# Kernel tuning notes

Measured on AMD Instinct MI355X. Metric: run time of the kernel, lower is better.

The kernel has to match this reference:

```python
import jax, jax.numpy as jnp
import numpy as np

D_MODEL, N_HEAD, D_FFN = 1024, 16, 4096
MAX_REL = 128
NUM_BUCKETS = 2 * MAX_REL - 1  # 255
B, T = 2, 2048


def algebraic_ln(x, gamma, beta, a, b_raw, eps=1e-5):
    mean = jnp.mean(x, axis=-1, keepdims=True)
    var = jnp.var(x, axis=-1, keepdims=True)  # unbiased=False
    z = var + eps
    b = jax.nn.softplus(10.0 * b_raw) / 10.0  # softplus with beta=10
    p = a[0] + a[1] * z + a[2] * z ** 2
    q = b[0] + b[1] * z + b[2] * z ** 2
    return (x - mean) * (p / q) * gamma + beta


def setup_inputs() -> dict:
    key = jax.random.key(0)
    ks = jax.random.split(key, 16)
    s = (1.0 / np.sqrt(D_MODEL)).astype(np.float32)
    inp = {
        'x': jax.random.normal(ks[0], (B, T, D_MODEL), jnp.float32),
        'casual_mask': jnp.tril(jnp.ones((T, T), dtype=bool)),
        'Wq': jax.random.normal(ks[1], (D_MODEL, D_MODEL), jnp.float32) * s,
        'bq': jnp.zeros((D_MODEL,), jnp.float32),
        'Wk': jax.random.normal(ks[2], (D_MODEL, D_MODEL), jnp.float32) * s,
        'bk': jnp.zeros((D_MODEL,), jnp.float32),
        'Wv': jax.random.normal(ks[3], (D_MODEL, D_MODEL), jnp.float32) * s,
        'bv': jnp.zeros((D_MODEL,), jnp.float32),
        'Wo': jax.random.normal(ks[4], (D_MODEL, D_MODEL), jnp.float32) * s,
        'bo': jnp.zeros((D_MODEL,), jnp.float32),
        'rel_emb': jax.random.normal(ks[5], (NUM_BUCKETS, N_HEAD), jnp.float32) * 0.02,
        'g1': jnp.ones((D_MODEL,), jnp.float32),
        'be1': jnp.zeros((D_MODEL,), jnp.float32),
        'a1': jnp.array([1.0, 0.5, 0.1], jnp.float32),
        'br1': jnp.array([1.0, 0.3, 0.05], jnp.float32),
        'g2': jnp.ones((D_MODEL,), jnp.float32),
        'be2': jnp.zeros((D_MODEL,), jnp.float32),
        'a2': jnp.array([1.0, 0.5, 0.1], jnp.float32),
        'br2': jnp.array([1.0, 0.3, 0.05], jnp.float32),
        'W1': jax.random.normal(ks[6], (D_FFN, D_MODEL), jnp.float32) * s,
        'b1': jnp.zeros((D_FFN,), jnp.float32),
        'W2': jax.random.normal(ks[7], (D_MODEL, D_FFN), jnp.float32) * (1.0 / np.sqrt(D_FFN)),
        'b2': jnp.zeros((D_MODEL,), jnp.float32),
        'res_scale': jnp.array(0.5, jnp.float32),
    }
    return inp


def attention(x, mask, Wq, bq, Wk, bk, Wv, bv, Wo, bo, rel_emb):
    Bx, Tx, C = x.shape
    H, Dh = N_HEAD, C // N_HEAD
    scale = Dh ** -0.5
    Q = (x @ Wq.T + bq).reshape(Bx, Tx, H, Dh)
    K = (x @ Wk.T + bk).reshape(Bx, Tx, H, Dh)
    V = (x @ Wv.T + bv).reshape(Bx, Tx, H, Dh)
    scores = jnp.einsum('bqhd,bkhd->bhqk', Q, K) * scale
    rel = jnp.arange(Tx)[None, :] - jnp.arange(Tx)[:, None]  # k_pos - q_pos
    buckets = jnp.clip(rel, -MAX_REL + 1, MAX_REL - 1) + (MAX_REL - 1)
    bias = rel_emb[buckets]  # [T,T,H]
    scores = scores + jnp.transpose(bias, (2, 0, 1))[None]
    m = mask[None, None]  # [1,1,T,T]
    # torch: masked_fill(-inf) then masked_fill(0) -> masked entries become 0
    scores = jnp.where(m, scores, 0.0)
    w = jax.nn.relu(scores) + 1e-6
    w = jnp.where(m, w, 0.0)
    w = w / (jnp.sum(w, axis=-1, keepdims=True) + 1e-6)
    out = jnp.einsum('bhqk,bkhd->bqhd', w, V).reshape(Bx, Tx, C)
    return out @ Wo.T + bo


def reference(x, casual_mask, Wq, bq, Wk, bk, Wv, bv, Wo, bo, rel_emb,
              g1, be1, a1, br1, g2, be2, a2, br2, W1, b1, W2, b2, res_scale):
    scale = jnp.clip(res_scale, 0.2, 1.0)
    x = x + scale * attention(algebraic_ln(x, g1, be1, a1, br1), casual_mask,
                              Wq, bq, Wk, bk, Wv, bv, Wo, bo, rel_emb)
    h = algebraic_ln(x, g2, be2, a2, br2)
    ffn = jax.nn.relu(h @ W1.T + b1) @ W2.T + b2  # dropout is identity at eval
    return x + scale * ffn
```

## Files before the change

kernel.cpp:

```cpp
#include <hip/hip_runtime.h>
#include <stdint.h>


#define D_MODEL 1024
#define T_SEQ   2048
#define NHEAD   16
#define DH      64
#define DFFN    4096
#define MROWS   4096

using short8  = __attribute__((ext_vector_type(8))) short;
using floatx4 = __attribute__((ext_vector_type(4))) float;

__device__ __forceinline__ float bf2f(ushort u) {
    union { uint32_t i; float f; } x; x.i = ((uint32_t)u) << 16; return x.f;
}
__device__ __forceinline__ ushort f2bf(float f) {
    union { float f; uint32_t i; } x; x.f = f;
    uint32_t i = x.i;
    return (ushort)((i + 0x7fffu + ((i >> 16) & 1u)) >> 16);
}
__device__ __forceinline__ float ldf(const void* p, size_t i, int dt) {
    return dt ? bf2f(((const ushort*)p)[i]) : ((const float*)p)[i];
}
__device__ __forceinline__ int detect_bf16(const void* g1) {
    return *(const uint32_t*)g1 == 0x3F803F80u;
}
__device__ __forceinline__ void gld_lds16(const void* g, void* l) {
    __builtin_amdgcn_global_load_lds(
        (__attribute__((address_space(1))) uint32_t*)(g),
        (__attribute__((address_space(3))) uint32_t*)(l), 16, 0, 0);
}
__device__ __forceinline__ float softplus10(float t) {
    float u = 10.f * t;
    return (u > 20.f ? u : log1pf(expf(u))) * 0.1f;
}

template <int INMODE>
__global__ __launch_bounds__(256)
void ln_kernel(const void* __restrict__ xin,
               const void* __restrict__ gamma, const void* __restrict__ beta,
               const void* __restrict__ a3, const void* __restrict__ br3,
               ushort* __restrict__ out, const void* __restrict__ dtprobe)
{
    const int dt = detect_bf16(dtprobe);
    const int row = blockIdx.x;
    const int tid = threadIdx.x;
    const int col = tid * 4;
    float v[4];
    if (INMODE == 1) {
        const float* x = (const float*)xin + (size_t)row * D_MODEL;
        float4 t = *(const float4*)(x + col);
        v[0] = t.x; v[1] = t.y; v[2] = t.z; v[3] = t.w;
    } else if (dt) {
        const ushort* x = (const ushort*)xin + (size_t)row * D_MODEL;
        ushort4 t = *(const ushort4*)(x + col);
        v[0] = bf2f(t.x); v[1] = bf2f(t.y); v[2] = bf2f(t.z); v[3] = bf2f(t.w);
    } else {
        const float* x = (const float*)xin + (size_t)row * D_MODEL;
        float4 t = *(const float4*)(x + col);
        v[0] = t.x; v[1] = t.y; v[2] = t.z; v[3] = t.w;
    }
    float s  = v[0] + v[1] + v[2] + v[3];
    float s2 = v[0]*v[0] + v[1]*v[1] + v[2]*v[2] + v[3]*v[3];
#pragma unroll
    for (int m = 32; m > 0; m >>= 1) {
        s  += __shfl_down(s,  m, 64);
        s2 += __shfl_down(s2, m, 64);
    }
    __shared__ float wsum[4], wsum2[4];
    const int wave = tid >> 6, lane = tid & 63;
    if (lane == 0) { wsum[wave] = s; wsum2[wave] = s2; }
    __syncthreads();
    s  = wsum[0] + wsum[1] + wsum[2] + wsum[3];
    s2 = wsum2[0] + wsum2[1] + wsum2[2] + wsum2[3];
    const float mean = s * (1.f / D_MODEL);
    const float var  = s2 * (1.f / D_MODEL) - mean * mean;
    const float z = var + 1e-5f;
    const float a0 = ldf(a3, 0, dt), a1 = ldf(a3, 1, dt), a2 = ldf(a3, 2, dt);
    const float b0 = softplus10(ldf(br3, 0, dt));
    const float b1 = softplus10(ldf(br3, 1, dt));
    const float b2 = softplus10(ldf(br3, 2, dt));
    const float p = a0 + a1 * z + a2 * z * z;
    const float q = b0 + b1 * z + b2 * z * z;
    const float f = p / q;
    ushort4 o; ushort* op = (ushort*)&o;
#pragma unroll
    for (int e = 0; e < 4; e++) {
        op[e] = f2bf((v[e] - mean) * f * ldf(gamma, col + e, dt) + ldf(beta, col + e, dt));
    }
    *(ushort4*)(out + (size_t)row * D_MODEL + col) = o;
}

template <int MODE, int BM, int BN>
__global__ __launch_bounds__(256)
void gemm_bt(const ushort* __restrict__ A,
             const void* __restrict__ Bw0, const void* __restrict__ Bw1,
             const void* __restrict__ Bw2,
             const void* __restrict__ bias0, const void* __restrict__ bias1,
             const void* __restrict__ bias2,
             void* __restrict__ C0, void* __restrict__ C1, void* __restrict__ C2v,
             int Nst, int K, const void* __restrict__ dtprobe)
{
    constexpr int NI = BM / 32;
    constexpr int NJ = BN / 32;
    constexpr int AC = BM / 64;
    constexpr int BC = BN / 64;
    __shared__ __align__(16) ushort As[BM * 32];
    __shared__ __align__(16) ushort Bs[BN * 32];
    const int dt = detect_bf16(dtprobe);
    const int tid  = threadIdx.x;
    const int wave = tid >> 6, lane = tid & 63;
    const int wr = wave >> 1, wc = wave & 1;
    const int g = lane >> 4, l15 = lane & 15;

    const void* Bw = Bw0; const void* bias = bias0; void* Cout = C0;
    if (MODE == 4) {
        const int mat = blockIdx.x >> 3;
        if (mat == 1)      { Bw = Bw1; bias = bias1; Cout = C1; }
        else if (mat == 2) { Bw = Bw2; bias = bias2; Cout = C2v; }
    }
    const int m0 = blockIdx.y * BM;
    const int n0 = (MODE == 4) ? ((blockIdx.x & 7) * 128) : (blockIdx.x * BN);

    floatx4 acc[NI][NJ];
#pragma unroll
    for (int i = 0; i < NI; i++)
#pragma unroll
        for (int j = 0; j < NJ; j++) acc[i][j] = {0.f, 0.f, 0.f, 0.f};

    const int srow = lane >> 2;
    const int ssw  = (srow >> 1) & 3;
    const int scol = (((lane & 3) ^ ssw) * 8);
    const int fsw  = (l15 >> 1) & 3;
    for (int k0 = 0; k0 < K; k0 += 32) {
        __syncthreads();
        if (dt) {
            const ushort* Bb = (const ushort*)Bw;
#pragma unroll
            for (int c = 0; c < AC; c++) {
                const int r0 = (wave * AC + c) * 16;
                gld_lds16(A + (size_t)(m0 + r0 + srow) * K + k0 + scol, &As[r0 * 32]);
            }
#pragma unroll
            for (int c = 0; c < BC; c++) {
                const int r0 = (wave * BC + c) * 16;
                gld_lds16(Bb + (size_t)(n0 + r0 + srow) * K + k0 + scol, &Bs[r0 * 32]);
            }
        } else {
            const float* Bf = (const float*)Bw;
#pragma unroll
            for (int c = 0; c < AC; c++) {
                const int r0 = (wave * AC + c) * 16;
                gld_lds16(A + (size_t)(m0 + r0 + srow) * K + k0 + scol, &As[r0 * 32]);
            }
#pragma unroll
            for (int c = 0; c < BC; c++) {
                const int r0 = (wave * BC + c) * 16;
                const float* src = Bf + (size_t)(n0 + r0 + srow) * K + k0 + scol;
                float4 t0 = *(const float4*)(src);
                float4 t1 = *(const float4*)(src + 4);
                ushort tmp[8] = { f2bf(t0.x), f2bf(t0.y), f2bf(t0.z), f2bf(t0.w),
                                  f2bf(t1.x), f2bf(t1.y), f2bf(t1.z), f2bf(t1.w) };
                *(short8*)&Bs[(r0 + srow) * 32 + (lane & 3) * 8] = *(short8*)tmp;
            }
        }
        __syncthreads();
        short8 af[NI], bfr[NJ];
#pragma unroll
        for (int i = 0; i < NI; i++)
            af[i]  = *(const short8*)&As[(wr * (BM / 2) + i * 16 + l15) * 32 + ((g ^ fsw) * 8)];
#pragma unroll
        for (int j = 0; j < NJ; j++)
            bfr[j] = *(const short8*)&Bs[(wc * (BN / 2) + j * 16 + l15) * 32 + ((g ^ fsw) * 8)];
#pragma unroll
        for (int i = 0; i < NI; i++)
#pragma unroll
            for (int j = 0; j < NJ; j++)
                acc[i][j] = __builtin_amdgcn_mfma_f32_16x16x32_bf16(af[i], bfr[j], acc[i][j], 0, 0, 0);
    }

#pragma unroll
    for (int i = 0; i < NI; i++) {
        const int rowb = m0 + wr * (BM / 2) + i * 16 + g * 4;
#pragma unroll
        for (int j = 0; j < NJ; j++) {
            const int col = n0 + wc * (BN / 2) + j * 16 + l15;
            const float bi = ldf(bias, col, dt);
#pragma unroll
            for (int r = 0; r < 4; r++) {
                const size_t idx = (size_t)(rowb + r) * Nst + col;
                const float v = acc[i][j][r] + bi;
                if (MODE == 1) ((ushort*)Cout)[idx] = f2bf(fmaxf(v, 0.f));
                else           ((ushort*)Cout)[idx] = f2bf(v);
            }
        }
    }
}

template <int MODE>
__global__ __launch_bounds__(256)
void gemm_k64c(const ushort* __restrict__ A, const void* __restrict__ Bw,
               const void* __restrict__ bias, void* __restrict__ Cout,
               const void* __restrict__ resid, const void* __restrict__ scale_p,
               int Nst, int K, const void* __restrict__ dtprobe)
{
    __shared__ __align__(16) ushort As[2][2][64 * 32];
    __shared__ __align__(16) ushort Bs[2][2][64 * 32];
    const int dt = detect_bf16(dtprobe);
    const int tid  = threadIdx.x;
    const int wave = tid >> 6, lane = tid & 63;
    const int wr = wave >> 1, wc = wave & 1;
    const int g = lane >> 4, l15 = lane & 15;
    const int m0 = blockIdx.y * 64, n0 = blockIdx.x * 64;

    floatx4 acc[2][2];
#pragma unroll
    for (int i = 0; i < 2; i++)
#pragma unroll
        for (int j = 0; j < 2; j++) acc[i][j] = {0.f, 0.f, 0.f, 0.f};

    const int srow = lane >> 2;
    const int ssw  = (srow >> 1) & 3;
    const int scol = (((lane & 3) ^ ssw) * 8);
    const int fsw  = (l15 >> 1) & 3;
    const int r0   = wave * 16;

    const int nt = K >> 6;
    int cur = 0;

    if (dt) {
        const ushort* Bb = (const ushort*)Bw;
        auto stage_dt = [&](int buf, int k0) {
#pragma unroll
            for (int kb = 0; kb < 2; kb++) {
                gld_lds16(A  + (size_t)(m0 + r0 + srow) * K + k0 + kb * 32 + scol, &As[buf][kb][r0 * 32]);
                gld_lds16(Bb + (size_t)(n0 + r0 + srow) * K + k0 + kb * 32 + scol, &Bs[buf][kb][r0 * 32]);
            }
        };
        stage_dt(0, 0);
        asm volatile("s_waitcnt vmcnt(0)" ::: "memory");
        __builtin_amdgcn_sched_barrier(0);
        __builtin_amdgcn_s_barrier();
        for (int t = 0; t < nt; ++t) {
            if (t + 1 < nt) {
                stage_dt(cur ^ 1, (t + 1) << 6);
                asm volatile("s_waitcnt vmcnt(4)" ::: "memory");
            } else {
                asm volatile("s_waitcnt vmcnt(0)" ::: "memory");
            }
            __builtin_amdgcn_sched_barrier(0);
            __builtin_amdgcn_s_barrier();
            short8 af[2][2], bfr[2][2];
#pragma unroll
            for (int kb = 0; kb < 2; kb++) {
#pragma unroll
                for (int i = 0; i < 2; i++)
                    af[i][kb]  = *(const short8*)&As[cur][kb][(wr * 32 + i * 16 + l15) * 32 + ((g ^ fsw) * 8)];
#pragma unroll
                for (int j = 0; j < 2; j++)
                    bfr[j][kb] = *(const short8*)&Bs[cur][kb][(wc * 32 + j * 16 + l15) * 32 + ((g ^ fsw) * 8)];
            }
#pragma unroll
            for (int kb = 0; kb < 2; kb++)
#pragma unroll
                for (int i = 0; i < 2; i++)
#pragma unroll
                    for (int j = 0; j < 2; j++)
                        acc[i][j] = __builtin_amdgcn_mfma_f32_16x16x32_bf16(af[i][kb], bfr[j][kb], acc[i][j], 0, 0, 0);
            __builtin_amdgcn_s_barrier();
            cur ^= 1;
        }
    } else {
        const float* Bf = (const float*)Bw;
        auto stage_f = [&](int buf, int k0) {
#pragma unroll
            for (int kb = 0; kb < 2; kb++) {
                gld_lds16(A + (size_t)(m0 + r0 + srow) * K + k0 + kb * 32 + scol, &As[buf][kb][r0 * 32]);
                const float* src = Bf + (size_t)(n0 + r0 + srow) * K + k0 + kb * 32 + scol;
                float4 t0 = *(const float4*)(src);
                float4 t1 = *(const float4*)(src + 4);
                ushort tmp[8] = { f2bf(t0.x), f2bf(t0.y), f2bf(t0.z), f2bf(t0.w),
                                  f2bf(t1.x), f2bf(t1.y), f2bf(t1.z), f2bf(t1.w) };
                *(short8*)&Bs[buf][kb][(r0 + srow) * 32 + (lane & 3) * 8] = *(short8*)tmp;
            }
        };
        stage_f(0, 0);
        __syncthreads();
        for (int t = 0; t < nt; ++t) {
            if (t + 1 < nt) stage_f(cur ^ 1, (t + 1) << 6);
            short8 af[2][2], bfr[2][2];
#pragma unroll
            for (int kb = 0; kb < 2; kb++) {
#pragma unroll
                for (int i = 0; i < 2; i++)
                    af[i][kb]  = *(const short8*)&As[cur][kb][(wr * 32 + i * 16 + l15) * 32 + ((g ^ fsw) * 8)];
#pragma unroll
                for (int j = 0; j < 2; j++)
                    bfr[j][kb] = *(const short8*)&Bs[cur][kb][(wc * 32 + j * 16 + l15) * 32 + ((g ^ fsw) * 8)];
            }
#pragma unroll
            for (int kb = 0; kb < 2; kb++)
#pragma unroll
                for (int i = 0; i < 2; i++)
#pragma unroll
                    for (int j = 0; j < 2; j++)
                        acc[i][j] = __builtin_amdgcn_mfma_f32_16x16x32_bf16(af[i][kb], bfr[j][kb], acc[i][j], 0, 0, 0);
            __syncthreads();
            cur ^= 1;
        }
    }

    const float scl = fminf(fmaxf(ldf(scale_p, 0, dt), 0.2f), 1.0f);
#pragma unroll
    for (int i = 0; i < 2; i++) {
        const int rowb = m0 + wr * 32 + i * 16 + g * 4;
#pragma unroll
        for (int j = 0; j < 2; j++) {
            const int col = n0 + wc * 32 + j * 16 + l15;
            const float bi = ldf(bias, col, dt);
#pragma unroll
            for (int r = 0; r < 4; r++) {
                const size_t idx = (size_t)(rowb + r) * Nst + col;
                const float v = acc[i][j][r] + bi;
                if (MODE == 2) ((float*)Cout)[idx] = ldf(resid, idx, dt) + scl * v;
                else {
                    const float o = ((const float*)resid)[idx] + scl * v;
                    if (dt) ((ushort*)Cout)[idx] = f2bf(o);
                    else    ((float*)Cout)[idx]  = o;
                }
            }
        }
    }
}

__global__ __launch_bounds__(256)
void attn_kernel(const ushort* __restrict__ Q, const ushort* __restrict__ K,
                 const ushort* __restrict__ V, const void* __restrict__ rel,
                 ushort* __restrict__ Out, const void* __restrict__ dtprobe)
{
    __shared__ __align__(16) ushort Ks[64 * 64];
    __shared__ __align__(16) ushort Vt[64 * 88];
    __shared__ __align__(16) ushort Ss[64 * 88];
    __shared__ float rel_h[128];
    __shared__ float den_l[64];

    const int dt = detect_bf16(dtprobe);
    const int tid  = threadIdx.x;
    const int wave = tid >> 6, lane = tid & 63;
    const int wr = wave >> 1, wc = wave & 1;
    const int g = lane >> 4, l15 = lane & 15;
    const int pair = blockIdx.x, h = blockIdx.y, b = blockIdx.z;

    if (tid < 128) rel_h[tid] = ldf(rel, (size_t)tid * NHEAD + h, dt);
    const float scale = 0.125f;

    for (int ph = 0; ph < 2; ph++) {
        const int qt = ph ? (31 - pair) : pair;
        __syncthreads();
        if (tid < 64) den_l[tid] = 0.f;

        const ushort* Qg = Q + ((size_t)(b * T_SEQ + qt * 64)) * D_MODEL + h * DH;
        short8 qa[2][2];
#pragma unroll
        for (int i = 0; i < 2; i++)
#pragma unroll
            for (int ks = 0; ks < 2; ks++)
                qa[i][ks] = *(const short8*)(Qg + (size_t)(wr * 32 + i * 16 + l15) * D_MODEL
                                             + (ks * 4 + g) * 8);

        floatx4 onum[2][2];
#pragma unroll
        for (int i = 0; i < 2; i++) { onum[i][0] = {0.f,0.f,0.f,0.f}; onum[i][1] = {0.f,0.f,0.f,0.f}; }
        float den_p[2][4];
#pragma unroll
        for (int i = 0; i < 2; i++)
#pragma unroll
            for (int r = 0; r < 4; r++) den_p[i][r] = 0.f;

        const int nk = qt + 1;
        for (int kt = 0; kt < nk; kt++) {
            const int kbase = kt * 64;
            __syncthreads();
            const ushort* Kg = K + ((size_t)(b * T_SEQ + kbase)) * D_MODEL + h * DH;
            {
                const int lrow = lane >> 3, pch = lane & 7;
#pragma unroll
                for (int c = 0; c < 2; c++) {
                    const int r0 = (wave * 2 + c) * 8;
                    const int row = r0 + lrow;
                    gld_lds16(Kg + (size_t)row * D_MODEL + ((pch ^ (row & 7)) * 8), &Ks[r0 * 64]);
                }
            }
            const ushort* Vg = V + ((size_t)(b * T_SEQ + kbase)) * D_MODEL + h * DH;
#pragma unroll
            for (int c = 0; c < 2; c++) {
                const int chunk = tid + c * 256;
                const int krow = chunk >> 3;
                const int bb   = chunk & 7;
                short8 t = *(const short8*)(Vg + (size_t)krow * D_MODEL + bb * 8);
                ushort tmp[8]; *(short8*)tmp = t;
#pragma unroll
                for (int e = 0; e < 8; e++) {
                    const int ee = (e + bb) & 7;
                    Vt[(bb * 8 + ee) * 88 + krow] = tmp[ee];
                }
            }
            __syncthreads();

            floatx4 sacc[2][2];
#pragma unroll
            for (int i = 0; i < 2; i++) { sacc[i][0] = {0.f,0.f,0.f,0.f}; sacc[i][1] = {0.f,0.f,0.f,0.f}; }
#pragma unroll
            for (int ks = 0; ks < 2; ks++) {
                short8 kb[2];
                const int ch = ks * 4 + g;
#pragma unroll
                for (int j = 0; j < 2; j++) {
                    const int row = wc * 32 + j * 16 + l15;
                    kb[j] = *(const short8*)&Ks[row * 64 + ((ch ^ (row & 7)) * 8)];
                }
#pragma unroll
                for (int i = 0; i < 2; i++)
#pragma unroll
                    for (int j = 0; j < 2; j++)
                        sacc[i][j] = __builtin_amdgcn_mfma_f32_16x16x32_bf16(qa[i][ks], kb[j], sacc[i][j], 0, 0, 0);
            }

            const int dq = qt - kt;
            if (dq >= 3) {
                const float c0 = rel_h[0];
#pragma unroll
                for (int i = 0; i < 2; i++) {
                    const int qrow = wr * 32 + i * 16 + g * 4;
#pragma unroll
                    for (int j = 0; j < 2; j++) {
                        const int kcol = wc * 32 + j * 16 + l15;
#pragma unroll
                        for (int r = 0; r < 4; r++) {
                            const float w = fmaxf(sacc[i][j][r] * scale + c0, 0.f) + 1e-6f;
                            den_p[i][r] += w;
                            Ss[(qrow + r) * 88 + kcol] = f2bf(w);
                        }
                    }
                }
            } else {
#pragma unroll
                for (int i = 0; i < 2; i++) {
                    const int qrow = wr * 32 + i * 16 + g * 4;
#pragma unroll
                    for (int j = 0; j < 2; j++) {
                        const int kcol = wc * 32 + j * 16 + l15;
                        const int kg = kbase + kcol;
#pragma unroll
                        for (int r = 0; r < 4; r++) {
                            const int qg = qt * 64 + qrow + r;
                            const int d = qg - kg;
                            float w = 0.f;
                            if (d >= 0) {
                                const int bucket = 127 - (d < 127 ? d : 127);
                                const float sv = sacc[i][j][r] * scale + rel_h[bucket];
                                w = fmaxf(sv, 0.f) + 1e-6f;
                            }
                            den_p[i][r] += w;
                            Ss[(qrow + r) * 88 + kcol] = f2bf(w);
                        }
                    }
                }
            }
            __syncthreads();

#pragma unroll
            for (int ks = 0; ks < 2; ks++) {
                short8 wa[2], vb[2];
#pragma unroll
                for (int i = 0; i < 2; i++)
                    wa[i] = *(const short8*)&Ss[(wr * 32 + i * 16 + l15) * 88 + ks * 32 + g * 8];
#pragma unroll
                for (int j = 0; j < 2; j++)
                    vb[j] = *(const short8*)&Vt[(wc * 32 + j * 16 + l15) * 88 + ks * 32 + g * 8];
#pragma unroll
                for (int i = 0; i < 2; i++)
#pragma unroll
                    for (int j = 0; j < 2; j++)
                        onum[i][j] = __builtin_amdgcn_mfma_f32_16x16x32_bf16(wa[i], vb[j], onum[i][j], 0, 0, 0);
            }
        }

#pragma unroll
        for (int i = 0; i < 2; i++)
#pragma unroll
            for (int r = 0; r < 4; r++) {
                float v = den_p[i][r];
                v += __shfl_xor(v, 1, 64);
                v += __shfl_xor(v, 2, 64);
                v += __shfl_xor(v, 4, 64);
                v += __shfl_xor(v, 8, 64);
                den_p[i][r] = v;
            }
        __syncthreads();
        if (l15 == 0) {
#pragma unroll
            for (int i = 0; i < 2; i++)
#pragma unroll
                for (int r = 0; r < 4; r++)
                    atomicAdd(&den_l[wr * 32 + i * 16 + g * 4 + r], den_p[i][r]);
        }
        __syncthreads();

        const size_t obase = ((size_t)(b * T_SEQ + qt * 64)) * D_MODEL + h * DH;
#pragma unroll
        for (int i = 0; i < 2; i++) {
            const int qrow = wr * 32 + i * 16 + g * 4;
#pragma unroll
            for (int j = 0; j < 2; j++) {
                const int dcol = wc * 32 + j * 16 + l15;
#pragma unroll
                for (int r = 0; r < 4; r++) {
                    const float dn = den_l[qrow + r] + 1e-6f;
                    Out[obase + (size_t)(qrow + r) * D_MODEL + dcol] = f2bf(onum[i][j][r] / dn);
                }
            }
        }
    }
}

extern "C" void kernel_launch(void* const* d_in, const int* in_sizes, int n_in,
                              void* d_out, int out_size, void* d_ws, size_t ws_size,
                              hipStream_t stream)
{
    const void* x   = d_in[0];
    const void* Wq  = d_in[2];
    const void* bq  = d_in[3];
    const void* Wk  = d_in[4];
    const void* bk  = d_in[5];
    const void* Wv  = d_in[6];
    const void* bv  = d_in[7];
    const void* Wo  = d_in[8];
    const void* bo  = d_in[9];
    const void* rel = d_in[10];
    const void* g1  = d_in[11];
    const void* be1 = d_in[12];
    const void* a1  = d_in[13];
    const void* br1 = d_in[14];
    const void* g2  = d_in[15];
    const void* be2 = d_in[16];
    const void* a2  = d_in[17];
    const void* br2 = d_in[18];
    const void* W1  = d_in[19];
    const void* b1  = d_in[20];
    const void* W2  = d_in[21];
    const void* b2  = d_in[22];
    const void* rs  = d_in[23];

    char* ws = (char*)d_ws;
    ushort* ln1  = (ushort*)(ws);
    ushort* Qb   = (ushort*)(ws + (8u  << 20));
    ushort* Kb   = (ushort*)(ws + (16u << 20));
    ushort* Vb   = (ushort*)(ws + (24u << 20));
    ushort* atb  = (ushort*)(ws + (32u << 20));
    float*  x1   = (float*)(ws + (40u << 20));
    ushort* hbuf = (ushort*)(ws + (56u << 20));
    ushort* ffn1 = (ushort*)(ws);

    const dim3 blk(256);

    ln_kernel<0><<<dim3(MROWS), blk, 0, stream>>>(x, g1, be1, a1, br1, ln1, g1);
    gemm_bt<4, 128, 128><<<dim3(24, MROWS / 128), blk, 0, stream>>>(
        ln1, Wq, Wk, Wv, bq, bk, bv, Qb, Kb, Vb, D_MODEL, D_MODEL, g1);
    attn_kernel<<<dim3(16, NHEAD, 2), blk, 0, stream>>>(Qb, Kb, Vb, rel, atb, g1);
    gemm_k64c<2><<<dim3(D_MODEL / 64, MROWS / 64), blk, 0, stream>>>(
        atb, Wo, bo, x1, x, rs, D_MODEL, D_MODEL, g1);
    ln_kernel<1><<<dim3(MROWS), blk, 0, stream>>>(x1, g2, be2, a2, br2, hbuf, g1);
    gemm_bt<1, 128, 128><<<dim3(DFFN / 128, MROWS / 128), blk, 0, stream>>>(
        hbuf, W1, nullptr, nullptr, b1, nullptr, nullptr, ffn1, nullptr, nullptr,
        DFFN, D_MODEL, g1);
    gemm_k64c<3><<<dim3(D_MODEL / 64, MROWS / 64), blk, 0, stream>>>(
        ffn1, W2, b2, d_out, x1, rs, D_MODEL, DFFN, g1);
}
```

Baseline: 494.3 us.

## Double-buffer LDS tiles in the bt GEMM to overlap loads with MFMA

Turns the shared-memory A/B tiles of the QKV and FFN1 GEMM into two ping-pong buffers. While one tile feeds MFMA, the next K-slice is fetched into the other. Partial vmcnt waits and raw s_barrier calls replace the two __syncthreads per iteration. This is meant to hide global-load latency behind compute, at the cost of twice the LDS per block (which may lower occupancy) and fragile hand-written waitcnt logic.

```diff
diff --git a/kernel.cpp b/kernel.cpp
--- a/kernel.cpp
+++ b/kernel.cpp
@@ -94,20 +94,20 @@
 
 template <int MODE, int BM, int BN>
 __global__ __launch_bounds__(256)
-void gemm_bt(const ushort* __restrict__ A,
-             const void* __restrict__ Bw0, const void* __restrict__ Bw1,
-             const void* __restrict__ Bw2,
-             const void* __restrict__ bias0, const void* __restrict__ bias1,
-             const void* __restrict__ bias2,
-             void* __restrict__ C0, void* __restrict__ C1, void* __restrict__ C2v,
-             int Nst, int K, const void* __restrict__ dtprobe)
+void gemm_btc(const ushort* __restrict__ A,
+              const void* __restrict__ Bw0, const void* __restrict__ Bw1,
+              const void* __restrict__ Bw2,
+              const void* __restrict__ bias0, const void* __restrict__ bias1,
+              const void* __restrict__ bias2,
+              void* __restrict__ C0, void* __restrict__ C1, void* __restrict__ C2v,
+              int Nst, int K, const void* __restrict__ dtprobe)
 {
     constexpr int NI = BM / 32;
     constexpr int NJ = BN / 32;
     constexpr int AC = BM / 64;
     constexpr int BC = BN / 64;
-    __shared__ __align__(16) ushort As[BM * 32];
-    __shared__ __align__(16) ushort Bs[BN * 32];
+    __shared__ __align__(16) ushort As[2][BM * 32];
+    __shared__ __align__(16) ushort Bs[2][BN * 32];
     const int dt = detect_bf16(dtprobe);
     const int tid  = threadIdx.x;
     const int wave = tid >> 6, lane = tid & 63;
@@ -133,26 +133,58 @@
     const int ssw  = (srow >> 1) & 3;
     const int scol = (((lane & 3) ^ ssw) * 8);
     const int fsw  = (l15 >> 1) & 3;
-    for (int k0 = 0; k0 < K; k0 += 32) {
-        __syncthreads();
-        if (dt) {
-            const ushort* Bb = (const ushort*)Bw;
+    const int nt = K >> 5;
+    int cur = 0;
+
+    if (dt) {
+        const ushort* Bb = (const ushort*)Bw;
+        auto stage_dt = [&](int buf, int k0) {
 #pragma unroll
             for (int c = 0; c < AC; c++) {
                 const int r0 = (wave * AC + c) * 16;
-                gld_lds16(A + (size_t)(m0 + r0 + srow) * K + k0 + scol, &As[r0 * 32]);
+                gld_lds16(A + (size_t)(m0 + r0 + srow) * K + k0 + scol, &As[buf][r0 * 32]);
             }
 #pragma unroll
             for (int c = 0; c < BC; c++) {
                 const int r0 = (wave * BC + c) * 16;
-                gld_lds16(Bb + (size_t)(n0 + r0 + srow) * K + k0 + scol, &Bs[r0 * 32]);
-            }
-        } else {
-            const float* Bf = (const float*)Bw;
+                gld_lds16(Bb + (size_t)(n0 + r0 + srow) * K + k0 + scol, &Bs[buf][r0 * 32]);
+            }
+        };
+        stage_dt(0, 0);
+        asm volatile("s_waitcnt vmcnt(0)" ::: "memory");
+        __builtin_amdgcn_sched_barrier(0);
+        __builtin_amdgcn_s_barrier();
+        for (int t = 0; t < nt; ++t) {
+            if (t + 1 < nt) {
+                stage_dt(cur ^ 1, (t + 1) << 5);
+                asm volatile("s_waitcnt vmcnt(4)" ::: "memory");
+            } else {
+                asm volatile("s_waitcnt vmcnt(0)" ::: "memory");
+            }
+            __builtin_amdgcn_sched_barrier(0);
+            __builtin_amdgcn_s_barrier();
+            short8 af[NI], bfr[NJ];
+#pragma unroll
+            for (int i = 0; i < NI; i++)
+                af[i]  = *(const short8*)&As[cur][(wr * (BM / 2) + i * 16 + l15) * 32 + ((g ^ fsw) * 8)];
+#pragma unroll
+            for (int j = 0; j < NJ; j++)
+                bfr[j] = *(const short8*)&Bs[cur][(wc * (BN / 2) + j * 16 + l15) * 32 + ((g ^ fsw) * 8)];
+#pragma unroll
+            for (int i = 0; i < NI; i++)
+#pragma unroll
+                for (int j = 0; j < NJ; j++)
+                    acc[i][j] = __builtin_amdgcn_mfma_f32_16x16x32_bf16(af[i], bfr[j], acc[i][j], 0, 0, 0);
+            __builtin_amdgcn_s_barrier();
+            cur ^= 1;
+        }
+    } else {
+        const float* Bf = (const float*)Bw;
+        auto stage_f = [&](int buf, int k0) {
 #pragma unroll
             for (int c = 0; c < AC; c++) {
                 const int r0 = (wave * AC + c) * 16;
-                gld_lds16(A + (size_t)(m0 + r0 + srow) * K + k0 + scol, &As[r0 * 32]);
+                gld_lds16(A + (size_t)(m0 + r0 + srow) * K + k0 + scol, &As[buf][r0 * 32]);
             }
 #pragma unroll
             for (int c = 0; c < BC; c++) {
@@ -162,22 +194,28 @@
                 float4 t1 = *(const float4*)(src + 4);
                 ushort tmp[8] = { f2bf(t0.x), f2bf(t0.y), f2bf(t0.z), f2bf(t0.w),
                                   f2bf(t1.x), f2bf(t1.y), f2bf(t1.z), f2bf(t1.w) };
-                *(short8*)&Bs[(r0 + srow) * 32 + (lane & 3) * 8] = *(short8*)tmp;
-            }
-        }
+                *(short8*)&Bs[buf][(r0 + srow) * 32 + (lane & 3) * 8] = *(short8*)tmp;
+            }
+        };
+        stage_f(0, 0);
         __syncthreads();
-        short8 af[NI], bfr[NJ];
-#pragma unroll
-        for (int i = 0; i < NI; i++)
-            af[i]  = *(const short8*)&As[(wr * (BM / 2) + i * 16 + l15) * 32 + ((g ^ fsw) * 8)];
-#pragma unroll
-        for (int j = 0; j < NJ; j++)
-            bfr[j] = *(const short8*)&Bs[(wc * (BN / 2) + j * 16 + l15) * 32 + ((g ^ fsw) * 8)];
-#pragma unroll
-        for (int i = 0; i < NI; i++)
+        for (int t = 0; t < nt; ++t) {
+            if (t + 1 < nt) stage_f(cur ^ 1, (t + 1) << 5);
+            short8 af[NI], bfr[NJ];
+#pragma unroll
+            for (int i = 0; i < NI; i++)
+                af[i]  = *(const short8*)&As[cur][(wr * (BM / 2) + i * 16 + l15) * 32 + ((g ^ fsw) * 8)];
 #pragma unroll
             for (int j = 0; j < NJ; j++)
-                acc[i][j] = __builtin_amdgcn_mfma_f32_16x16x32_bf16(af[i], bfr[j], acc[i][j], 0, 0, 0);
+                bfr[j] = *(const short8*)&Bs[cur][(wc * (BN / 2) + j * 16 + l15) * 32 + ((g ^ fsw) * 8)];
+#pragma unroll
+            for (int i = 0; i < NI; i++)
+#pragma unroll
+                for (int j = 0; j < NJ; j++)
+                    acc[i][j] = __builtin_amdgcn_mfma_f32_16x16x32_bf16(af[i], bfr[j], acc[i][j], 0, 0, 0);
+            __syncthreads();
+            cur ^= 1;
+        }
     }
 
 #pragma unroll
@@ -566,13 +604,13 @@
     const dim3 blk(256);
 
     ln_kernel<0><<<dim3(MROWS), blk, 0, stream>>>(x, g1, be1, a1, br1, ln1, g1);
-    gemm_bt<4, 128, 128><<<dim3(24, MROWS / 128), blk, 0, stream>>>(
+    gemm_btc<4, 128, 128><<<dim3(24, MROWS / 128), blk, 0, stream>>>(
         ln1, Wq, Wk, Wv, bq, bk, bv, Qb, Kb, Vb, D_MODEL, D_MODEL, g1);
     attn_kernel<<<dim3(16, NHEAD, 2), blk, 0, stream>>>(Qb, Kb, Vb, rel, atb, g1);
     gemm_k64c<2><<<dim3(D_MODEL / 64, MROWS / 64), blk, 0, stream>>>(
         atb, Wo, bo, x1, x, rs, D_MODEL, D_MODEL, g1);
     ln_kernel<1><<<dim3(MROWS), blk, 0, stream>>>(x1, g2, be2, a2, br2, hbuf, g1);
-    gemm_bt<1, 128, 128><<<dim3(DFFN / 128, MROWS / 128), blk, 0, stream>>>(
+    gemm_btc<1, 128, 128><<<dim3(DFFN / 128, MROWS / 128), blk, 0, stream>>>(
         hbuf, W1, nullptr, nullptr, b1, nullptr, nullptr, ffn1, nullptr, nullptr,
         DFFN, D_MODEL, g1);
     gemm_k64c<3><<<dim3(D_MODEL / 64, MROWS / 64), blk, 0, stream>>>(
```

After: 481.9 us, median of 3. 2.5% less time.
